# Performance work log

Measured on AMD Instinct MI355X. Metric: run time of the kernel, lower is better.

## Reference

```python
import jax, jax.numpy as jnp
import numpy as np

D_MODEL, N_HEADS, D_STATE, N_GROUPS, CHUNK = 2048, 32, 64, 1, 256
BATCH, SEQLEN = 2, 4096


def setup_inputs() -> dict:
    key = jax.random.key(0)
    ks = jax.random.split(key, 8)
    s = 0.02
    d, h, n, g = D_MODEL, N_HEADS, D_STATE, N_GROUPS
    return {
        "x": jax.random.normal(ks[0], (BATCH, SEQLEN, d), jnp.float32),
        "A_log": jnp.log(jnp.arange(1, h + 1, dtype=jnp.float32)),
        "D": jnp.ones((h,), jnp.float32),
        "B_w": jax.random.normal(ks[1], (g * n, d), jnp.float32) * s,
        "B_b": jnp.zeros((g * n,), jnp.float32),
        "C_w": jax.random.normal(ks[2], (g * n, d), jnp.float32) * s,
        "C_b": jnp.zeros((g * n,), jnp.float32),
        "dt_w": jax.random.normal(ks[3], (h, d), jnp.float32) * s,
        "dt_b": jnp.zeros((h,), jnp.float32),
        "out_w": jax.random.normal(ks[4], (d, d), jnp.float32) * s,
        "out_b": jnp.zeros((d,), jnp.float32),
    }


def segsum(v):
    # v: [..., T] -> [..., T, T]; out[i,j] = sum_{k=j+1..i} v[k] for i>=j, -inf else
    cs = jnp.cumsum(v, axis=-1)
    seg = cs[..., :, None] - cs[..., None, :]
    T = v.shape[-1]
    mask = jnp.tril(jnp.ones((T, T), bool))
    return jnp.where(mask, seg, -jnp.inf)


def _ssd(x, A_log, D, B_w, B_b, C_w, C_b, dt_w, dt_b, out_w, out_b):
    b, t, d = x.shape
    h = A_log.shape[0]
    n = B_w.shape[0] // N_GROUPS
    p = d // h
    l = CHUNK
    c = t // l

    A = -jnp.exp(A_log.astype(jnp.float32))                      # [h]
    B = (x @ B_w.T + B_b).reshape(b, t, N_GROUPS, n)             # g=1
    C = (x @ C_w.T + C_b).reshape(b, t, N_GROUPS, n)
    B = jnp.broadcast_to(B, (b, t, h, n))                        # repeat groups -> heads
    C = jnp.broadcast_to(C, (b, t, h, n))
    dt = jax.nn.softplus(x @ dt_w.T + dt_b)                      # [b,t,h]
    xh = x.reshape(b, t, h, p)

    # chunked SSD (Mamba2 mamba_chunk_scan_combined math)
    xc = xh.reshape(b, c, l, h, p)
    Bc = B.reshape(b, c, l, h, n)
    Cc = C.reshape(b, c, l, h, n)
    dtc = dt.reshape(b, c, l, h)
    dA = jnp.transpose(dtc * A, (0, 3, 1, 2))                    # [b,h,c,l]
    A_cumsum = jnp.cumsum(dA, axis=-1)                           # [b,h,c,l]

    # 1. intra-chunk (diagonal blocks)
    L = jnp.exp(segsum(dA))                                      # [b,h,c,l,l]
    xdt = xc * dtc[..., None]                                    # [b,c,l,h,p]
    Y_diag = jnp.einsum('bclhn,bcshn,bhcls,bcshp->bclhp', Cc, Bc, L, xdt)

    # 2. per-chunk final states
    decay_states = jnp.exp(A_cumsum[..., -1:] - A_cumsum)        # [b,h,c,l]
    states = jnp.einsum('bclhn,bhcl,bclhp->bchpn', Bc, decay_states, xdt)

    # 3. inter-chunk recurrence on chunk states
    states = jnp.concatenate([jnp.zeros_like(states[:, :1]), states], axis=1)  # [b,c+1,h,p,n]
    dA_last = jnp.pad(A_cumsum[..., -1], ((0, 0), (0, 0), (1, 0)))             # [b,h,c+1]
    decay_chunk = jnp.exp(segsum(dA_last))                                     # [b,h,c+1,c+1]
    new_states = jnp.einsum('bhzc,bchpn->bzhpn', decay_chunk, states)
    prev_states = new_states[:, :-1]                                           # [b,c,h,p,n]

    # 4. state -> output contribution
    state_decay_out = jnp.exp(A_cumsum)                          # [b,h,c,l]
    Y_off = jnp.einsum('bclhn,bchpn,bhcl->bclhp', Cc, prev_states, state_decay_out)

    Y = (Y_diag + Y_off).reshape(b, t, h, p) + D[None, None, :, None] * xh
    return Y.reshape(b, t, d) @ out_w.T + out_b


def reference(x, A_log, D, B_w, B_b, C_w, C_b, dt_w, dt_b, out_w, out_b):
    return _ssd(x, A_log, D, B_w, B_b, C_w, C_b, dt_w, dt_b, out_w, out_b)
```

## Files before the change

kernel.cpp:

```cpp
#include <hip/hip_runtime.h>
#include <hip/hip_bf16.h>
#include <math.h>

namespace {
constexpr int kDModel = 2048;
constexpr int kHeads  = 32;
constexpr int kState  = 64;
constexpr int kP      = 64;
constexpr int kChunk  = 256;
constexpr int kNChunk = 16;
constexpr int kBatch  = 2;
constexpr int kSeq    = 4096;
constexpr int kM      = kBatch * kSeq;
}

typedef __bf16 bf16_t;
typedef __attribute__((ext_vector_type(8))) __bf16 bf16x8;
typedef __attribute__((ext_vector_type(4))) __bf16 bf16x4;
typedef __attribute__((ext_vector_type(4))) float f32x4;

__device__ __forceinline__ void gload_lds16(const void* g, void* l) {
    __builtin_amdgcn_global_load_lds(
        (const __attribute__((address_space(1))) void*)g,
        (__attribute__((address_space(3))) void*)l,
        16, 0, 0);
}

__global__ __launch_bounds__(256)
void gemm_bcdt(const bf16_t* __restrict__ A, const bf16_t* __restrict__ W,
               const float* __restrict__ b0, const float* __restrict__ b1,
               const float* __restrict__ b2,
               bf16_t* __restrict__ o0h, bf16_t* __restrict__ o1h,
               float* __restrict__ o2f)
{
    constexpr int K = kDModel;
    __shared__ __bf16 AstS[64 * 32];
    __shared__ __bf16 WstS[128 * 32];
    const int tid  = threadIdx.x;
    const int lane = tid & 63;
    const int wave = tid >> 6;
    const int wm = (wave >> 1) * 32;
    const int wn = (wave & 1) * 64;
    const int l15 = lane & 15, quad = lane >> 4;
    const int m0 = blockIdx.y * 64;
    const int n0 = blockIdx.x * 128;
    const int u0 = tid, u1 = tid + 256;

    f32x4 acc[2][4];
    #pragma unroll
    for (int i = 0; i < 2; ++i)
        #pragma unroll
        for (int j = 0; j < 4; ++j)
            acc[i][j] = (f32x4){0.f, 0.f, 0.f, 0.f};

    for (int k0 = 0; k0 < K; k0 += 32) {
        gload_lds16(A + (size_t)(m0 + (tid >> 2)) * K + k0 + (tid & 3) * 8, AstS + tid * 8);
        gload_lds16(W + (size_t)(n0 + (u0 >> 2)) * K + k0 + (u0 & 3) * 8, WstS + u0 * 8);
        gload_lds16(W + (size_t)(n0 + (u1 >> 2)) * K + k0 + (u1 & 3) * 8, WstS + u1 * 8);
        __syncthreads();
        bf16x8 af[2], bfr[4];
        #pragma unroll
        for (int mi = 0; mi < 2; ++mi)
            af[mi] = *reinterpret_cast<const bf16x8*>(&AstS[(wm + mi * 16 + l15) * 32 + quad * 8]);
        #pragma unroll
        for (int ni = 0; ni < 4; ++ni)
            bfr[ni] = *reinterpret_cast<const bf16x8*>(&WstS[(wn + ni * 16 + l15) * 32 + quad * 8]);
        #pragma unroll
        for (int mi = 0; mi < 2; ++mi)
            #pragma unroll
            for (int ni = 0; ni < 4; ++ni)
                acc[mi][ni] = __builtin_amdgcn_mfma_f32_16x16x32_bf16(
                    af[mi], bfr[ni], acc[mi][ni], 0, 0, 0);
        __syncthreads();
    }

    #pragma unroll
    for (int mi = 0; mi < 2; ++mi) {
        #pragma unroll
        for (int reg = 0; reg < 4; ++reg) {
            const int r = m0 + wm + mi * 16 + quad * 4 + reg;
            #pragma unroll
            for (int ni = 0; ni < 4; ++ni) {
                const float v = acc[mi][ni][reg];
                const int n = n0 + wn + ni * 16 + l15;
                if (n < 64) {
                    o0h[(size_t)r * 64 + n] = (bf16_t)(v + b0[n]);
                } else if (n < 128) {
                    o1h[(size_t)r * 64 + (n - 64)] = (bf16_t)(v + b1[n - 64]);
                } else if (n < 160) {
                    float z = v + b2[n - 128];
                    o2f[(size_t)r * 32 + (n - 128)] = (z > 20.f) ? z : log1pf(expf(z));
                }
            }
        }
    }
}

__global__ __launch_bounds__(512, 2)
void gemm256_out(const bf16_t* __restrict__ Ap, const bf16_t* __restrict__ Bp,
                 const float* __restrict__ bias, float* __restrict__ C)
{
    constexpr int M = 8192, N = 2048, NT = 2048 / 32;
    __shared__ __bf16 Ab[3][4 * 256 * 8];
    __shared__ __bf16 Bb[3][4 * 256 * 8];
    const int tid  = threadIdx.x;
    const int lane = tid & 63;
    const int wave = tid >> 6;
    const int l15 = lane & 15, quad = lane >> 4;
    const int bid = blockIdx.x;
    const int mt = (bid & 7) * 4 + ((bid >> 3) & 3);
    const int nt = bid >> 5;
    const int m0 = mt * 256;
    const int n0 = nt * 256;
    const int wm = (wave >> 2) * 128;
    const int wn = (wave & 3) * 64;

    const int u0 = tid, u1 = tid + 512;
    auto stage = [&](int t2, int stb) {
        const int ks0 = t2 * 4;
        const bf16_t* As = Ap + ((size_t)ks0 * M + m0) * 8;
        const bf16_t* Bs = Bp + ((size_t)ks0 * N + n0) * 8;
        __bf16* Al = &Ab[stb][0];
        __bf16* Bl = &Bb[stb][0];
        gload_lds16(As + ((size_t)(u0 >> 8) * M + (u0 & 255)) * 8, Al + u0 * 8);
        gload_lds16(As + ((size_t)(u1 >> 8) * M + (u1 & 255)) * 8, Al + u1 * 8);
        gload_lds16(Bs + ((size_t)(u0 >> 8) * N + (u0 & 255)) * 8, Bl + u0 * 8);
        gload_lds16(Bs + ((size_t)(u1 >> 8) * N + (u1 & 255)) * 8, Bl + u1 * 8);
    };

    f32x4 acc[8][4];
    #pragma unroll
    for (int i = 0; i < 8; ++i)
        #pragma unroll
        for (int j = 0; j < 4; ++j)
            acc[i][j] = (f32x4){0.f, 0.f, 0.f, 0.f};

    stage(0, 0);
    stage(1, 1);
    asm volatile("s_waitcnt vmcnt(4)" ::: "memory");
    __builtin_amdgcn_s_barrier();

    int cur = 0;
    for (int t = 0; t < NT; ++t) {
        const __bf16* Ac = &Ab[cur][0];
        const __bf16* Bc = &Bb[cur][0];
        int stb = cur + 2; if (stb >= 3) stb -= 3;

        bf16x8 af[4], bfr[4];
        #pragma unroll
        for (int mi = 0; mi < 4; ++mi)
            af[mi] = *reinterpret_cast<const bf16x8*>(
                &Ac[(quad * 256 + wm + mi * 16 + l15) * 8]);
        #pragma unroll
        for (int nj = 0; nj < 4; ++nj)
            bfr[nj] = *reinterpret_cast<const bf16x8*>(
                &Bc[(quad * 256 + wn + nj * 16 + l15) * 8]);
        if (t < NT - 2) stage(t + 2, stb);
        __builtin_amdgcn_s_setprio(1);
        #pragma unroll
        for (int mi = 0; mi < 4; ++mi)
            #pragma unroll
            for (int nj = 0; nj < 4; ++nj)
                acc[mi][nj] = __builtin_amdgcn_mfma_f32_16x16x32_bf16(
                    af[mi], bfr[nj], acc[mi][nj], 0, 0, 0);
        __builtin_amdgcn_s_setprio(0);

        #pragma unroll
        for (int mi = 0; mi < 4; ++mi)
            af[mi] = *reinterpret_cast<const bf16x8*>(
                &Ac[(quad * 256 + wm + 64 + mi * 16 + l15) * 8]);
        __builtin_amdgcn_s_setprio(1);
        #pragma unroll
        for (int mi = 0; mi < 4; ++mi)
            #pragma unroll
            for (int nj = 0; nj < 4; ++nj)
                acc[4 + mi][nj] = __builtin_amdgcn_mfma_f32_16x16x32_bf16(
                    af[mi], bfr[nj], acc[4 + mi][nj], 0, 0, 0);
        __builtin_amdgcn_s_setprio(0);

        if (t < NT - 2) {
            asm volatile("s_waitcnt vmcnt(4)" ::: "memory");
        } else if (t < NT - 1) {
            asm volatile("s_waitcnt vmcnt(0)" ::: "memory");
        }
        if (t < NT - 1) __builtin_amdgcn_s_barrier();
        cur = cur + 1; if (cur == 3) cur = 0;
    }

    float bia[4];
    #pragma unroll
    for (int nj = 0; nj < 4; ++nj) bia[nj] = bias[n0 + wn + nj * 16 + l15];
    #pragma unroll
    for (int mi = 0; mi < 8; ++mi) {
        #pragma unroll
        for (int reg = 0; reg < 4; ++reg) {
            const int r = m0 + wm + mi * 16 + quad * 4 + reg;
            #pragma unroll
            for (int nj = 0; nj < 4; ++nj) {
                const int c = n0 + wn + nj * 16 + l15;
                C[(size_t)r * N + c] = acc[mi][nj][reg] + bia[nj];
            }
        }
    }
}

__global__ __launch_bounds__(256)
void prep_fused(const float* __restrict__ x, bf16_t* __restrict__ xb,
                const float* __restrict__ W, bf16_t* __restrict__ Wp,
                const float* __restrict__ B_w, const float* __restrict__ C_w,
                const float* __restrict__ dt_w, bf16_t* __restrict__ wcat)
{
    const int bid = blockIdx.x;
    if (bid < 16384) {
        const int i = (bid * 256 + threadIdx.x) * 4;
        const float4 v = *reinterpret_cast<const float4*>(x + i);
        xb[i + 0] = (bf16_t)v.x;
        xb[i + 1] = (bf16_t)v.y;
        xb[i + 2] = (bf16_t)v.z;
        xb[i + 3] = (bf16_t)v.w;
    } else if (bid < 16384 + 2048) {
        const int idx = (bid - 16384) * 256 + threadIdx.x;
        const int n = idx >> 8, ks = idx & 255;
        const float4 v0 = *reinterpret_cast<const float4*>(W + (size_t)n * 2048 + ks * 8);
        const float4 v1 = *reinterpret_cast<const float4*>(W + (size_t)n * 2048 + ks * 8 + 4);
        bf16x8 o;
        o[0] = (__bf16)v0.x; o[1] = (__bf16)v0.y; o[2] = (__bf16)v0.z; o[3] = (__bf16)v0.w;
        o[4] = (__bf16)v1.x; o[5] = (__bf16)v1.y; o[6] = (__bf16)v1.z; o[7] = (__bf16)v1.w;
        *reinterpret_cast<bf16x8*>(Wp + ((size_t)ks * 2048 + n) * 8) = o;
    } else {
        const int idx = (bid - 16384 - 2048) * 256 + threadIdx.x;
        const int r = idx >> 11, k = idx & 2047;
        float v = 0.f;
        if (r < 64)       v = B_w[r * 2048 + k];
        else if (r < 128) v = C_w[(r - 64) * 2048 + k];
        else if (r < 160) v = dt_w[(r - 128) * 2048 + k];
        wcat[idx] = (bf16_t)v;
    }
}

__global__ __launch_bounds__(kChunk)
void dtcumsum_kernel(const float* __restrict__ dtm, const float* __restrict__ A_log,
                     float* __restrict__ Acs)
{
    const int blk = blockIdx.x;
    const int ci = blk & (kNChunk - 1);
    const int hi = (blk >> 4) & (kHeads - 1);
    const int bi = blk >> 9;
    const int t = threadIdx.x;
    const float Ah = -expf(A_log[hi]);
    __shared__ float s[kChunk];
    s[t] = dtm[((size_t)bi * kSeq + ci * kChunk + t) * kHeads + hi] * Ah;
    __syncthreads();
    for (int off = 1; off < kChunk; off <<= 1) {
        const float add = (t >= off) ? s[t - off] : 0.f;
        __syncthreads();
        s[t] += add;
        __syncthreads();
    }
    Acs[((size_t)(bi * kHeads + hi) * kNChunk + ci) * kChunk + t] = s[t];
}

__global__ __launch_bounds__(256)
void bT_kernel(const bf16_t* __restrict__ Bb16, bf16_t* __restrict__ bTg)
{
    const int ci = blockIdx.x & (kNChunk - 1);
    const int bi = blockIdx.x >> 4;
    const size_t rowbase = (size_t)bi * kSeq + ci * kChunk;
    __shared__ __bf16 T[64 * 264];
    const int tid = threadIdx.x;
    bf16x8 v[8];
    #pragma unroll
    for (int e = 0; e < 8; ++e)
        v[e] = *reinterpret_cast<const bf16x8*>(Bb16 + (rowbase + tid) * 64 + e * 8);
    #pragma unroll
    for (int e = 0; e < 8; ++e)
        #pragma unroll
        for (int j = 0; j < 8; ++j)
            T[(e * 8 + j) * 264 + tid] = v[e][j];
    __syncthreads();
    const int n = tid >> 2, seg = (tid & 3) * 64;
    bf16_t* dst = bTg + ((size_t)(bi * kNChunk + ci)) * (64 * 256) + n * 256 + seg;
    #pragma unroll
    for (int j = 0; j < 8; ++j) {
        *reinterpret_cast<bf16x8*>(dst + j * 8) =
            *reinterpret_cast<const bf16x8*>(&T[n * 264 + seg + j * 8]);
    }
}

__global__ __launch_bounds__(256)
void xdtT_kernel(const bf16_t* __restrict__ xb, const float* __restrict__ dtm,
                 bf16_t* __restrict__ xdtT)
{
    const int blk = blockIdx.x;
    const int hi = blk & (kHeads - 1);
    const int ci = (blk >> 5) & (kNChunk - 1);
    const int bi = blk >> 9;
    const size_t rowbase = (size_t)bi * kSeq + ci * kChunk;
    __shared__ __bf16 T[64 * 264];
    const int tid = threadIdx.x;
    const float d = dtm[(rowbase + tid) * kHeads + hi];
    bf16x8 v[8];
    #pragma unroll
    for (int e = 0; e < 8; ++e)
        v[e] = *reinterpret_cast<const bf16x8*>(xb + (rowbase + tid) * kDModel + hi * kP + e * 8);
    #pragma unroll
    for (int e = 0; e < 8; ++e)
        #pragma unroll
        for (int j = 0; j < 8; ++j)
            T[(e * 8 + j) * 264 + tid] = (__bf16)((float)v[e][j] * d);
    __syncthreads();
    const int p = tid >> 2, seg = (tid & 3) * 64;
    bf16_t* dst = xdtT + (size_t)blk * (64 * 256) + p * 256 + seg;
    #pragma unroll
    for (int j = 0; j < 8; ++j) {
        *reinterpret_cast<bf16x8*>(dst + j * 8) =
            *reinterpret_cast<const bf16x8*>(&T[p * 264 + seg + j * 8]);
    }
}

__global__ __launch_bounds__(256)
void states_mfma(const bf16_t* __restrict__ xdtT, const bf16_t* __restrict__ bTg,
                 const float* __restrict__ Acs, float* __restrict__ states)
{
    const int blk = blockIdx.x;
    const int hi = blk & (kHeads - 1);
    const int ci = (blk >> 5) & (kNChunk - 1);
    const int bi = blk >> 9;
    __shared__ __bf16 Xa[64 * 264];
    __shared__ __bf16 Bt[64 * 264];
    __shared__ float dec[kChunk];
    const int tid = threadIdx.x;
    const int lane = tid & 63;
    const int wave = tid >> 6;
    const int l15 = lane & 15, quad = lane >> 4;

    const float* acs = Acs + ((size_t)(bi * kHeads + hi) * kNChunk + ci) * kChunk;
    dec[tid] = expf(acs[kChunk - 1] - acs[tid]);
    __syncthreads();

    const bf16_t* bsrc = bTg + ((size_t)(bi * kNChunk + ci)) * (64 * 256);
    const bf16_t* xsrc = xdtT + (size_t)blk * (64 * 256);
    #pragma unroll
    for (int e = 0; e < 8; ++e) {
        const int u = e * 256 + tid;
        const int r = u >> 5, seg = (u & 31) * 8;
        *reinterpret_cast<bf16x8*>(&Bt[r * 264 + seg]) =
            *reinterpret_cast<const bf16x8*>(bsrc + r * 256 + seg);
        bf16x8 xv = *reinterpret_cast<const bf16x8*>(xsrc + r * 256 + seg);
        bf16x8 xo;
        #pragma unroll
        for (int j = 0; j < 8; ++j)
            xo[j] = (__bf16)((float)xv[j] * dec[seg + j]);
        *reinterpret_cast<bf16x8*>(&Xa[r * 264 + seg]) = xo;
    }
    __syncthreads();

    f32x4 acc[4];
    #pragma unroll
    for (int ni = 0; ni < 4; ++ni) acc[ni] = (f32x4){0.f, 0.f, 0.f, 0.f};
    #pragma unroll
    for (int kk = 0; kk < 8; ++kk) {
        const bf16x8 af = *reinterpret_cast<const bf16x8*>(
            &Xa[(wave * 16 + l15) * 264 + kk * 32 + quad * 8]);
        #pragma unroll
        for (int ni = 0; ni < 4; ++ni) {
            const bf16x8 bf = *reinterpret_cast<const bf16x8*>(
                &Bt[(ni * 16 + l15) * 264 + kk * 32 + quad * 8]);
            acc[ni] = __builtin_amdgcn_mfma_f32_16x16x32_bf16(af, bf, acc[ni], 0, 0, 0);
        }
    }
    float* sp = states + (size_t)blk * (kP * kState);
    #pragma unroll
    for (int reg = 0; reg < 4; ++reg) {
        const int p = wave * 16 + quad * 4 + reg;
        #pragma unroll
        for (int ni = 0; ni < 4; ++ni)
            sp[(size_t)p * kState + ni * 16 + l15] = acc[ni][reg];
    }
}

__global__ __launch_bounds__(256)
void chunkscan_kernel(const float* __restrict__ states, const float* __restrict__ Acs,
                      bf16_t* __restrict__ prevsb)
{
    const int q  = blockIdx.x & 15;
    const int hi = (blockIdx.x >> 4) & (kHeads - 1);
    const int bi = blockIdx.x >> 9;
    const int e  = q * 256 + threadIdx.x;
    __shared__ float ea[kNChunk];
    if (threadIdx.x < kNChunk)
        ea[threadIdx.x] = expf(Acs[((size_t)(bi * kHeads + hi) * kNChunk + threadIdx.x)
                                   * kChunk + kChunk - 1]);
    __syncthreads();
    float P = 0.f;
    prevsb[((size_t)(bi * kNChunk + 0) * kHeads + hi) * (kP * kState) + e] = (bf16_t)0.f;
    for (int c = 1; c < kNChunk; ++c) {
        P = fmaf(ea[c - 1], P,
                 states[((size_t)(bi * kNChunk + (c - 1)) * kHeads + hi) * (kP * kState) + e]);
        prevsb[((size_t)(bi * kNChunk + c) * kHeads + hi) * (kP * kState) + e] = (bf16_t)P;
    }
}

__global__ __launch_bounds__(256)
void ychunk_mfma(const bf16_t* __restrict__ Bb16, const bf16_t* __restrict__ Cb16,
                 const bf16_t* __restrict__ xdtT, const float* __restrict__ Acs,
                 const bf16_t* __restrict__ prevsb, const float* __restrict__ dtm,
                 const float* __restrict__ Dvec, bf16_t* __restrict__ Yp)
{
    const int blk = blockIdx.x;
    const int lt = blk & 3;
    const int hi = (blk >> 2) & (kHeads - 1);
    const int ci = (blk >> 7) & (kNChunk - 1);
    const int bi = blk >> 11;
    __shared__ float acs_s[kChunk];
    __shared__ float dts_s[64];
    __shared__ __bf16 Cs[64 * 72];
    __shared__ __bf16 Bs[64 * 72];
    __shared__ __bf16 Xt[64 * 72];
    __shared__ __bf16 Sp[64 * 72];
    const int tid = threadIdx.x;
    const int lane = tid & 63;
    const int wave = tid >> 6;
    const int l15 = lane & 15, quad = lane >> 4;
    const int mrow = wave * 16 + quad * 4;
    const size_t rowbase = (size_t)bi * kSeq + ci * kChunk;
    const bf16_t* xdsrc = xdtT + ((size_t)((bi * kNChunk + ci) * kHeads + hi)) * (64 * 256);

    acs_s[tid] = Acs[((size_t)(bi * kHeads + hi) * kNChunk + ci) * kChunk + tid];
    if (tid < 64) dts_s[tid] = dtm[(rowbase + lt * 64 + tid) * kHeads + hi];
    const bf16_t* pp = prevsb + ((size_t)(bi * kNChunk + ci) * kHeads + hi) * (kP * kState);
    #pragma unroll
    for (int e = 0; e < 2; ++e) {
        const int u = e * 256 + tid;
        const int r = u >> 3, seg = (u & 7) * 8;
        *reinterpret_cast<bf16x8*>(&Cs[r * 72 + seg]) =
            *reinterpret_cast<const bf16x8*>(Cb16 + (rowbase + lt * 64 + r) * 64 + seg);
        *reinterpret_cast<bf16x8*>(&Bs[r * 72 + seg]) =
            *reinterpret_cast<const bf16x8*>(pp + r * 64 + seg);
    }
    __syncthreads();

    bf16x8 af[2];
    af[0] = *reinterpret_cast<const bf16x8*>(&Cs[(wave * 16 + l15) * 72 + quad * 8]);
    af[1] = *reinterpret_cast<const bf16x8*>(&Cs[(wave * 16 + l15) * 72 + 32 + quad * 8]);

    f32x4 yacc[4];
    #pragma unroll
    for (int ni = 0; ni < 4; ++ni) yacc[ni] = (f32x4){0.f, 0.f, 0.f, 0.f};
    #pragma unroll
    for (int ni = 0; ni < 4; ++ni) {
        const bf16x8 b0 = *reinterpret_cast<const bf16x8*>(&Bs[(ni * 16 + l15) * 72 + quad * 8]);
        const bf16x8 b1 = *reinterpret_cast<const bf16x8*>(&Bs[(ni * 16 + l15) * 72 + 32 + quad * 8]);
        yacc[ni] = __builtin_amdgcn_mfma_f32_16x16x32_bf16(af[0], b0, yacc[ni], 0, 0, 0);
        yacc[ni] = __builtin_amdgcn_mfma_f32_16x16x32_bf16(af[1], b1, yacc[ni], 0, 0, 0);
    }
    {
        float es[4];
        #pragma unroll
        for (int reg = 0; reg < 4; ++reg) es[reg] = expf(acs_s[lt * 64 + mrow + reg]);
        #pragma unroll
        for (int ni = 0; ni < 4; ++ni)
            #pragma unroll
            for (int reg = 0; reg < 4; ++reg) yacc[ni][reg] *= es[reg];
    }

    for (int st = 0; st <= lt; ++st) {
        __syncthreads();
        #pragma unroll
        for (int e = 0; e < 2; ++e) {
            const int u = e * 256 + tid;
            const int r = u >> 3, seg = (u & 7) * 8;
            *reinterpret_cast<bf16x8*>(&Bs[r * 72 + seg]) =
                *reinterpret_cast<const bf16x8*>(Bb16 + (rowbase + st * 64 + r) * 64 + seg);
            *reinterpret_cast<bf16x8*>(&Xt[r * 72 + seg]) =
                *reinterpret_cast<const bf16x8*>(xdsrc + r * 256 + st * 64 + seg);
        }
        __syncthreads();
        f32x4 sacc[4];
        #pragma unroll
        for (int ni = 0; ni < 4; ++ni) sacc[ni] = (f32x4){0.f, 0.f, 0.f, 0.f};
        #pragma unroll
        for (int ni = 0; ni < 4; ++ni) {
            const bf16x8 b0 = *reinterpret_cast<const bf16x8*>(&Bs[(ni * 16 + l15) * 72 + quad * 8]);
            const bf16x8 b1 = *reinterpret_cast<const bf16x8*>(&Bs[(ni * 16 + l15) * 72 + 32 + quad * 8]);
            sacc[ni] = __builtin_amdgcn_mfma_f32_16x16x32_bf16(af[0], b0, sacc[ni], 0, 0, 0);
            sacc[ni] = __builtin_amdgcn_mfma_f32_16x16x32_bf16(af[1], b1, sacc[ni], 0, 0, 0);
        }
        #pragma unroll
        for (int reg = 0; reg < 4; ++reg) {
            const int l = lt * 64 + mrow + reg;
            const float al = acs_s[l];
            #pragma unroll
            for (int ni = 0; ni < 4; ++ni) {
                const int scol = ni * 16 + l15;
                const int sg = st * 64 + scol;
                float v = sacc[ni][reg] * expf(al - acs_s[sg]);
                if (st == lt && sg > l) v = 0.f;
                Sp[(mrow + reg) * 72 + scol] = (__bf16)v;
            }
        }
        asm volatile("s_waitcnt lgkmcnt(0)" ::: "memory");
        __builtin_amdgcn_sched_barrier(0);
        const bf16x8 as0 = *reinterpret_cast<const bf16x8*>(&Sp[(wave * 16 + l15) * 72 + quad * 8]);
        const bf16x8 as1 = *reinterpret_cast<const bf16x8*>(&Sp[(wave * 16 + l15) * 72 + 32 + quad * 8]);
        #pragma unroll
        for (int ni = 0; ni < 4; ++ni) {
            const bf16x8 x0 = *reinterpret_cast<const bf16x8*>(&Xt[(ni * 16 + l15) * 72 + quad * 8]);
            const bf16x8 x1 = *reinterpret_cast<const bf16x8*>(&Xt[(ni * 16 + l15) * 72 + 32 + quad * 8]);
            yacc[ni] = __builtin_amdgcn_mfma_f32_16x16x32_bf16(as0, x0, yacc[ni], 0, 0, 0);
            yacc[ni] = __builtin_amdgcn_mfma_f32_16x16x32_bf16(as1, x1, yacc[ni], 0, 0, 0);
        }
    }

    const float Dh = Dvec[hi];
    #pragma unroll
    for (int reg = 0; reg < 4; ++reg) {
        const int lrow = mrow + reg;
        const size_t tg = rowbase + lt * 64 + lrow;
        const float dinv = 1.f / dts_s[lrow];
        #pragma unroll
        for (int ni = 0; ni < 4; ++ni) {
            const int p = ni * 16 + l15;
            const float xv = (float)Xt[p * 72 + lrow] * dinv;
            const float v = yacc[ni][reg] + Dh * xv;
            Yp[((size_t)(hi * 8 + (p >> 3)) * (size_t)kM + tg) * 8 + (p & 7)] = (bf16_t)v;
        }
    }
}

extern "C" void kernel_launch(void* const* d_in, const int* in_sizes, int n_in,
                              void* d_out, int out_size, void* d_ws, size_t ws_size,
                              hipStream_t stream)
{
    (void)in_sizes; (void)n_in; (void)out_size; (void)ws_size;
    const float* x     = (const float*)d_in[0];
    const float* A_log = (const float*)d_in[1];
    const float* Dvec  = (const float*)d_in[2];
    const float* B_w   = (const float*)d_in[3];
    const float* B_b   = (const float*)d_in[4];
    const float* C_w   = (const float*)d_in[5];
    const float* C_b   = (const float*)d_in[6];
    const float* dt_w  = (const float*)d_in[7];
    const float* dt_b  = (const float*)d_in[8];
    const float* out_w = (const float*)d_in[9];
    const float* out_b = (const float*)d_in[10];
    float* out = (float*)d_out;

    float* ws = (float*)d_ws;
    float* dtm    = ws;
    float* Acs    = dtm + (size_t)kM * kHeads;
    float* states = Acs + (size_t)kBatch * kHeads * kNChunk * kChunk;
    bf16_t* prevsb = (bf16_t*)(states + (size_t)kBatch * kNChunk * kHeads * kP * kState);
    bf16_t* xb    = prevsb + (size_t)kBatch * kNChunk * kHeads * kP * kState;
    bf16_t* Y     = xb;
    bf16_t* Bb16  = xb + (size_t)kM * kDModel;
    bf16_t* Cb16  = Bb16 + (size_t)kM * kState;
    bf16_t* xdtT  = Cb16 + (size_t)kM * kState;
    bf16_t* bTg   = xdtT + (size_t)kM * kDModel;
    bf16_t* wcat  = bTg + (size_t)kBatch * kNChunk * kState * kChunk;
    bf16_t* wob   = wcat + (size_t)256 * kDModel;

    const dim3 blk(256);
    prep_fused<<<dim3(16384 + 2048 + 2048), blk, 0, stream>>>(
        x, xb, out_w, wob, B_w, C_w, dt_w, wcat);
    gemm_bcdt<<<dim3(2, kM / 64), blk, 0, stream>>>(xb, wcat, B_b, C_b, dt_b,
                                                    Bb16, Cb16, dtm);
    dtcumsum_kernel<<<dim3(kBatch * kHeads * kNChunk), dim3(kChunk), 0, stream>>>(dtm, A_log, Acs);
    bT_kernel<<<dim3(kBatch * kNChunk), blk, 0, stream>>>(Bb16, bTg);
    xdtT_kernel<<<dim3(kBatch * kNChunk * kHeads), blk, 0, stream>>>(xb, dtm, xdtT);
    states_mfma<<<dim3(kBatch * kNChunk * kHeads), blk, 0, stream>>>(xdtT, bTg, Acs, states);
    chunkscan_kernel<<<dim3(kBatch * kHeads * 16), blk, 0, stream>>>(states, Acs, prevsb);
    ychunk_mfma<<<dim3(kBatch * kNChunk * kHeads * 4), blk, 0, stream>>>(
        Bb16, Cb16, xdtT, Acs, prevsb, dtm, Dvec, Y);
    gemm256_out<<<dim3(256), dim3(512), 0, stream>>>(Y, wob, out_b, out);
}
```

Measured before the change: 353.3 us.

## Fold x bf16 conversion into consumers and merge mid-stage kernels

Drops the separate pass that converted x to a bf16 copy. The B/C/dt projection GEMM now loads fp32 x and converts it into LDS itself, using one 32-row tile that covers all 160 output columns, with no zero-padded weight rows. The xdt transpose reads fp32 x directly. The dt cumsum, B transpose and xdt transpose kernels are merged into one launch selected by block ID. This removes a full write and read of a bf16 copy of x plus two launches. The cost is fp32 x being read twice, a GEMM tile that loads its A operand synchronously through registers, and a single LDS layout shared by the three merged branches.

```diff
diff --git a/kernel.cpp b/kernel.cpp
--- a/kernel.cpp
+++ b/kernel.cpp
@@ -27,70 +27,68 @@
 }
 
 __global__ __launch_bounds__(256)
-void gemm_bcdt(const bf16_t* __restrict__ A, const bf16_t* __restrict__ W,
+void gemm_bcdt(const float* __restrict__ x, const bf16_t* __restrict__ W,
                const float* __restrict__ b0, const float* __restrict__ b1,
                const float* __restrict__ b2,
                bf16_t* __restrict__ o0h, bf16_t* __restrict__ o1h,
                float* __restrict__ o2f)
 {
     constexpr int K = kDModel;
-    __shared__ __bf16 AstS[64 * 32];
-    __shared__ __bf16 WstS[128 * 32];
+    __shared__ __bf16 AstS[32 * 32];
+    __shared__ __bf16 WstS[160 * 32];
     const int tid  = threadIdx.x;
     const int lane = tid & 63;
     const int wave = tid >> 6;
-    const int wm = (wave >> 1) * 32;
-    const int wn = (wave & 1) * 64;
+    const int wm = (wave >> 1) * 16;
+    const int wn = (wave & 1) * 80;
     const int l15 = lane & 15, quad = lane >> 4;
-    const int m0 = blockIdx.y * 64;
-    const int n0 = blockIdx.x * 128;
-    const int u0 = tid, u1 = tid + 256;
-
-    f32x4 acc[2][4];
-    #pragma unroll
-    for (int i = 0; i < 2; ++i)
-        #pragma unroll
-        for (int j = 0; j < 4; ++j)
-            acc[i][j] = (f32x4){0.f, 0.f, 0.f, 0.f};
+    const int m0 = blockIdx.x * 32;
+    const int ar = tid >> 3;
+    const int ac = (tid & 7) * 4;
+
+    f32x4 acc[5];
+    #pragma unroll
+    for (int j = 0; j < 5; ++j) acc[j] = (f32x4){0.f, 0.f, 0.f, 0.f};
 
     for (int k0 = 0; k0 < K; k0 += 32) {
-        gload_lds16(A + (size_t)(m0 + (tid >> 2)) * K + k0 + (tid & 3) * 8, AstS + tid * 8);
-        gload_lds16(W + (size_t)(n0 + (u0 >> 2)) * K + k0 + (u0 & 3) * 8, WstS + u0 * 8);
-        gload_lds16(W + (size_t)(n0 + (u1 >> 2)) * K + k0 + (u1 & 3) * 8, WstS + u1 * 8);
-        __syncthreads();
-        bf16x8 af[2], bfr[4];
-        #pragma unroll
-        for (int mi = 0; mi < 2; ++mi)
-            af[mi] = *reinterpret_cast<const bf16x8*>(&AstS[(wm + mi * 16 + l15) * 32 + quad * 8]);
-        #pragma unroll
-        for (int ni = 0; ni < 4; ++ni)
-            bfr[ni] = *reinterpret_cast<const bf16x8*>(&WstS[(wn + ni * 16 + l15) * 32 + quad * 8]);
-        #pragma unroll
-        for (int mi = 0; mi < 2; ++mi)
-            #pragma unroll
-            for (int ni = 0; ni < 4; ++ni)
-                acc[mi][ni] = __builtin_amdgcn_mfma_f32_16x16x32_bf16(
-                    af[mi], bfr[ni], acc[mi][ni], 0, 0, 0);
-        __syncthreads();
-    }
-
-    #pragma unroll
-    for (int mi = 0; mi < 2; ++mi) {
-        #pragma unroll
-        for (int reg = 0; reg < 4; ++reg) {
-            const int r = m0 + wm + mi * 16 + quad * 4 + reg;
-            #pragma unroll
-            for (int ni = 0; ni < 4; ++ni) {
-                const float v = acc[mi][ni][reg];
-                const int n = n0 + wn + ni * 16 + l15;
-                if (n < 64) {
-                    o0h[(size_t)r * 64 + n] = (bf16_t)(v + b0[n]);
-                } else if (n < 128) {
-                    o1h[(size_t)r * 64 + (n - 64)] = (bf16_t)(v + b1[n - 64]);
-                } else if (n < 160) {
-                    float z = v + b2[n - 128];
-                    o2f[(size_t)r * 32 + (n - 128)] = (z > 20.f) ? z : log1pf(expf(z));
-                }
+        const float4 av = *reinterpret_cast<const float4*>(
+            x + (size_t)(m0 + ar) * K + k0 + ac);
+        bf16x4 a4;
+        a4[0] = (__bf16)av.x; a4[1] = (__bf16)av.y;
+        a4[2] = (__bf16)av.z; a4[3] = (__bf16)av.w;
+        *reinterpret_cast<bf16x4*>(&AstS[ar * 32 + ac]) = a4;
+        #pragma unroll
+        for (int e = 0; e < 3; ++e) {
+            const int u = e * 256 + tid;
+            if (u < 640)
+                gload_lds16(W + (size_t)(u >> 2) * K + k0 + (u & 3) * 8, WstS + u * 8);
+        }
+        __syncthreads();
+        bf16x8 af, bfr[5];
+        af = *reinterpret_cast<const bf16x8*>(&AstS[(wm + l15) * 32 + quad * 8]);
+        #pragma unroll
+        for (int nf = 0; nf < 5; ++nf)
+            bfr[nf] = *reinterpret_cast<const bf16x8*>(&WstS[(wn + nf * 16 + l15) * 32 + quad * 8]);
+        #pragma unroll
+        for (int nf = 0; nf < 5; ++nf)
+            acc[nf] = __builtin_amdgcn_mfma_f32_16x16x32_bf16(af, bfr[nf], acc[nf], 0, 0, 0);
+        __syncthreads();
+    }
+
+    #pragma unroll
+    for (int reg = 0; reg < 4; ++reg) {
+        const int r = m0 + wm + quad * 4 + reg;
+        #pragma unroll
+        for (int nf = 0; nf < 5; ++nf) {
+            const float v = acc[nf][reg];
+            const int n = wn + nf * 16 + l15;
+            if (n < 64) {
+                o0h[(size_t)r * 64 + n] = (bf16_t)(v + b0[n]);
+            } else if (n < 128) {
+                o1h[(size_t)r * 64 + (n - 64)] = (bf16_t)(v + b1[n - 64]);
+            } else {
+                float z = v + b2[n - 128];
+                o2f[(size_t)r * 32 + (n - 128)] = (z > 20.f) ? z : log1pf(expf(z));
             }
         }
     }
@@ -205,21 +203,13 @@
 }
 
 __global__ __launch_bounds__(256)
-void prep_fused(const float* __restrict__ x, bf16_t* __restrict__ xb,
-                const float* __restrict__ W, bf16_t* __restrict__ Wp,
+void prep_fused(const float* __restrict__ W, bf16_t* __restrict__ Wp,
                 const float* __restrict__ B_w, const float* __restrict__ C_w,
                 const float* __restrict__ dt_w, bf16_t* __restrict__ wcat)
 {
     const int bid = blockIdx.x;
-    if (bid < 16384) {
-        const int i = (bid * 256 + threadIdx.x) * 4;
-        const float4 v = *reinterpret_cast<const float4*>(x + i);
-        xb[i + 0] = (bf16_t)v.x;
-        xb[i + 1] = (bf16_t)v.y;
-        xb[i + 2] = (bf16_t)v.z;
-        xb[i + 3] = (bf16_t)v.w;
-    } else if (bid < 16384 + 2048) {
-        const int idx = (bid - 16384) * 256 + threadIdx.x;
+    if (bid < 2048) {
+        const int idx = bid * 256 + threadIdx.x;
         const int n = idx >> 8, ks = idx & 255;
         const float4 v0 = *reinterpret_cast<const float4*>(W + (size_t)n * 2048 + ks * 8);
         const float4 v1 = *reinterpret_cast<const float4*>(W + (size_t)n * 2048 + ks * 8 + 4);
@@ -228,93 +218,92 @@
         o[4] = (__bf16)v1.x; o[5] = (__bf16)v1.y; o[6] = (__bf16)v1.z; o[7] = (__bf16)v1.w;
         *reinterpret_cast<bf16x8*>(Wp + ((size_t)ks * 2048 + n) * 8) = o;
     } else {
-        const int idx = (bid - 16384 - 2048) * 256 + threadIdx.x;
+        const int idx = (bid - 2048) * 256 + threadIdx.x;
         const int r = idx >> 11, k = idx & 2047;
-        float v = 0.f;
+        float v;
         if (r < 64)       v = B_w[r * 2048 + k];
         else if (r < 128) v = C_w[(r - 64) * 2048 + k];
-        else if (r < 160) v = dt_w[(r - 128) * 2048 + k];
+        else              v = dt_w[(r - 128) * 2048 + k];
         wcat[idx] = (bf16_t)v;
     }
 }
 
-__global__ __launch_bounds__(kChunk)
-void dtcumsum_kernel(const float* __restrict__ dtm, const float* __restrict__ A_log,
-                     float* __restrict__ Acs)
-{
-    const int blk = blockIdx.x;
-    const int ci = blk & (kNChunk - 1);
-    const int hi = (blk >> 4) & (kHeads - 1);
-    const int bi = blk >> 9;
-    const int t = threadIdx.x;
-    const float Ah = -expf(A_log[hi]);
-    __shared__ float s[kChunk];
-    s[t] = dtm[((size_t)bi * kSeq + ci * kChunk + t) * kHeads + hi] * Ah;
-    __syncthreads();
-    for (int off = 1; off < kChunk; off <<= 1) {
-        const float add = (t >= off) ? s[t - off] : 0.f;
-        __syncthreads();
-        s[t] += add;
-        __syncthreads();
-    }
-    Acs[((size_t)(bi * kHeads + hi) * kNChunk + ci) * kChunk + t] = s[t];
-}
-
 __global__ __launch_bounds__(256)
-void bT_kernel(const bf16_t* __restrict__ Bb16, bf16_t* __restrict__ bTg)
-{
-    const int ci = blockIdx.x & (kNChunk - 1);
-    const int bi = blockIdx.x >> 4;
-    const size_t rowbase = (size_t)bi * kSeq + ci * kChunk;
-    __shared__ __bf16 T[64 * 264];
+void mid_fused(const float* __restrict__ dtm, const float* __restrict__ A_log,
+               float* __restrict__ Acs, const bf16_t* __restrict__ Bb16,
+               bf16_t* __restrict__ bTg, const float* __restrict__ x,
+               bf16_t* __restrict__ xdtT)
+{
+    const int bid = blockIdx.x;
     const int tid = threadIdx.x;
-    bf16x8 v[8];
-    #pragma unroll
-    for (int e = 0; e < 8; ++e)
-        v[e] = *reinterpret_cast<const bf16x8*>(Bb16 + (rowbase + tid) * 64 + e * 8);
-    #pragma unroll
-    for (int e = 0; e < 8; ++e)
-        #pragma unroll
-        for (int j = 0; j < 8; ++j)
-            T[(e * 8 + j) * 264 + tid] = v[e][j];
-    __syncthreads();
-    const int n = tid >> 2, seg = (tid & 3) * 64;
-    bf16_t* dst = bTg + ((size_t)(bi * kNChunk + ci)) * (64 * 256) + n * 256 + seg;
-    #pragma unroll
-    for (int j = 0; j < 8; ++j) {
-        *reinterpret_cast<bf16x8*>(dst + j * 8) =
-            *reinterpret_cast<const bf16x8*>(&T[n * 264 + seg + j * 8]);
-    }
-}
-
-__global__ __launch_bounds__(256)
-void xdtT_kernel(const bf16_t* __restrict__ xb, const float* __restrict__ dtm,
-                 bf16_t* __restrict__ xdtT)
-{
-    const int blk = blockIdx.x;
-    const int hi = blk & (kHeads - 1);
-    const int ci = (blk >> 5) & (kNChunk - 1);
-    const int bi = blk >> 9;
-    const size_t rowbase = (size_t)bi * kSeq + ci * kChunk;
-    __shared__ __bf16 T[64 * 264];
-    const int tid = threadIdx.x;
-    const float d = dtm[(rowbase + tid) * kHeads + hi];
-    bf16x8 v[8];
-    #pragma unroll
-    for (int e = 0; e < 8; ++e)
-        v[e] = *reinterpret_cast<const bf16x8*>(xb + (rowbase + tid) * kDModel + hi * kP + e * 8);
-    #pragma unroll
-    for (int e = 0; e < 8; ++e)
-        #pragma unroll
-        for (int j = 0; j < 8; ++j)
-            T[(e * 8 + j) * 264 + tid] = (__bf16)((float)v[e][j] * d);
-    __syncthreads();
-    const int p = tid >> 2, seg = (tid & 3) * 64;
-    bf16_t* dst = xdtT + (size_t)blk * (64 * 256) + p * 256 + seg;
-    #pragma unroll
-    for (int j = 0; j < 8; ++j) {
-        *reinterpret_cast<bf16x8*>(dst + j * 8) =
-            *reinterpret_cast<const bf16x8*>(&T[p * 264 + seg + j * 8]);
+    if (bid < 1024) {
+        const int ci = bid & (kNChunk - 1);
+        const int hi = (bid >> 4) & (kHeads - 1);
+        const int bi = bid >> 9;
+        const float Ah = -expf(A_log[hi]);
+        __shared__ float s[kChunk];
+        s[tid] = dtm[((size_t)bi * kSeq + ci * kChunk + tid) * kHeads + hi] * Ah;
+        __syncthreads();
+        for (int off = 1; off < kChunk; off <<= 1) {
+            const float add = (tid >= off) ? s[tid - off] : 0.f;
+            __syncthreads();
+            s[tid] += add;
+            __syncthreads();
+        }
+        Acs[((size_t)(bi * kHeads + hi) * kNChunk + ci) * kChunk + tid] = s[tid];
+    } else if (bid < 1024 + 32) {
+        const int blk = bid - 1024;
+        const int ci = blk & (kNChunk - 1);
+        const int bi = blk >> 4;
+        const size_t rowbase = (size_t)bi * kSeq + ci * kChunk;
+        __shared__ __bf16 T[64 * 264];
+        bf16x8 v[8];
+        #pragma unroll
+        for (int e = 0; e < 8; ++e)
+            v[e] = *reinterpret_cast<const bf16x8*>(Bb16 + (rowbase + tid) * 64 + e * 8);
+        #pragma unroll
+        for (int e = 0; e < 8; ++e)
+            #pragma unroll
+            for (int j = 0; j < 8; ++j)
+                T[(e * 8 + j) * 264 + tid] = v[e][j];
+        __syncthreads();
+        const int n = tid >> 2, seg = (tid & 3) * 64;
+        bf16_t* dst = bTg + ((size_t)(bi * kNChunk + ci)) * (64 * 256) + n * 256 + seg;
+        #pragma unroll
+        for (int j = 0; j < 8; ++j) {
+            *reinterpret_cast<bf16x8*>(dst + j * 8) =
+                *reinterpret_cast<const bf16x8*>(&T[n * 264 + seg + j * 8]);
+        }
+    } else {
+        const int blk = bid - 1024 - 32;
+        const int hi = blk & (kHeads - 1);
+        const int ci = (blk >> 5) & (kNChunk - 1);
+        const int bi = blk >> 9;
+        const size_t rowbase = (size_t)bi * kSeq + ci * kChunk;
+        __shared__ __bf16 T[64 * 264];
+        const float d = dtm[(rowbase + tid) * kHeads + hi];
+        const float* xs = x + (rowbase + tid) * kDModel + hi * kP;
+        #pragma unroll
+        for (int e = 0; e < 8; ++e) {
+            const float4 a = *reinterpret_cast<const float4*>(xs + e * 8);
+            const float4 b = *reinterpret_cast<const float4*>(xs + e * 8 + 4);
+            T[(e * 8 + 0) * 264 + tid] = (__bf16)(a.x * d);
+            T[(e * 8 + 1) * 264 + tid] = (__bf16)(a.y * d);
+            T[(e * 8 + 2) * 264 + tid] = (__bf16)(a.z * d);
+            T[(e * 8 + 3) * 264 + tid] = (__bf16)(a.w * d);
+            T[(e * 8 + 4) * 264 + tid] = (__bf16)(b.x * d);
+            T[(e * 8 + 5) * 264 + tid] = (__bf16)(b.y * d);
+            T[(e * 8 + 6) * 264 + tid] = (__bf16)(b.z * d);
+            T[(e * 8 + 7) * 264 + tid] = (__bf16)(b.w * d);
+        }
+        __syncthreads();
+        const int p = tid >> 2, seg = (tid & 3) * 64;
+        bf16_t* dst = xdtT + (size_t)blk * (64 * 256) + p * 256 + seg;
+        #pragma unroll
+        for (int j = 0; j < 8; ++j) {
+            *reinterpret_cast<bf16x8*>(dst + j * 8) =
+                *reinterpret_cast<const bf16x8*>(&T[p * 264 + seg + j * 8]);
+        }
     }
 }
 
@@ -551,23 +540,20 @@
     float* Acs    = dtm + (size_t)kM * kHeads;
     float* states = Acs + (size_t)kBatch * kHeads * kNChunk * kChunk;
     bf16_t* prevsb = (bf16_t*)(states + (size_t)kBatch * kNChunk * kHeads * kP * kState);
-    bf16_t* xb    = prevsb + (size_t)kBatch * kNChunk * kHeads * kP * kState;
-    bf16_t* Y     = xb;
-    bf16_t* Bb16  = xb + (size_t)kM * kDModel;
+    bf16_t* Y     = prevsb + (size_t)kBatch * kNChunk * kHeads * kP * kState;
+    bf16_t* Bb16  = Y + (size_t)kM * kDModel;
     bf16_t* Cb16  = Bb16 + (size_t)kM * kState;
     bf16_t* xdtT  = Cb16 + (size_t)kM * kState;
     bf16_t* bTg   = xdtT + (size_t)kM * kDModel;
     bf16_t* wcat  = bTg + (size_t)kBatch * kNChunk * kState * kChunk;
-    bf16_t* wob   = wcat + (size_t)256 * kDModel;
+    bf16_t* wob   = wcat + (size_t)160 * kDModel;
 
     const dim3 blk(256);
-    prep_fused<<<dim3(16384 + 2048 + 2048), blk, 0, stream>>>(
-        x, xb, out_w, wob, B_w, C_w, dt_w, wcat);
-    gemm_bcdt<<<dim3(2, kM / 64), blk, 0, stream>>>(xb, wcat, B_b, C_b, dt_b,
-                                                    Bb16, Cb16, dtm);
-    dtcumsum_kernel<<<dim3(kBatch * kHeads * kNChunk), dim3(kChunk), 0, stream>>>(dtm, A_log, Acs);
-    bT_kernel<<<dim3(kBatch * kNChunk), blk, 0, stream>>>(Bb16, bTg);
-    xdtT_kernel<<<dim3(kBatch * kNChunk * kHeads), blk, 0, stream>>>(xb, dtm, xdtT);
+    prep_fused<<<dim3(2048 + 1280), blk, 0, stream>>>(out_w, wob, B_w, C_w, dt_w, wcat);
+    gemm_bcdt<<<dim3(kM / 32), blk, 0, stream>>>(x, wcat, B_b, C_b, dt_b,
+                                                 Bb16, Cb16, dtm);
+    mid_fused<<<dim3(1024 + 32 + 1024), blk, 0, stream>>>(
+        dtm, A_log, Acs, Bb16, bTg, x, xdtT);
     states_mfma<<<dim3(kBatch * kNChunk * kHeads), blk, 0, stream>>>(xdtT, bTg, Acs, states);
     chunkscan_kernel<<<dim3(kBatch * kHeads * 16), blk, 0, stream>>>(states, Acs, prevsb);
     ychunk_mfma<<<dim3(kBatch * kNChunk * kHeads * 4), blk, 0, stream>>>(
```

Result: no change. 356.3 us (+0.8%).
